# Kernel tuning notes

Measured on AMD Instinct MI355X. Metric: run time of the kernel, lower is better.

Reference implementation:

```python
import jax, jax.numpy as jnp
import numpy as np

EMBED_DIM = 1024
NUM_HEADS = 16
HEAD_DIM = EMBED_DIM // NUM_HEADS
B, T = 4, 2048


def setup_inputs() -> dict:
    key = jax.random.key(0)
    ks = jax.random.split(key, 10)
    s = 1.0 / np.sqrt(EMBED_DIM)
    inp = {
        "x": jax.random.normal(ks[0], (B, T, EMBED_DIM), dtype=jnp.float32),
        "mask": jnp.ones((B, T), dtype=bool),
        "q_w": jax.random.uniform(ks[1], (EMBED_DIM, EMBED_DIM), jnp.float32, -s, s),
        "q_b": jax.random.uniform(ks[2], (EMBED_DIM,), jnp.float32, -s, s),
        "k_w": jax.random.uniform(ks[3], (EMBED_DIM, EMBED_DIM), jnp.float32, -s, s),
        "k_b": jax.random.uniform(ks[4], (EMBED_DIM,), jnp.float32, -s, s),
        "v_w": jax.random.uniform(ks[5], (EMBED_DIM, EMBED_DIM), jnp.float32, -s, s),
        "v_b": jax.random.uniform(ks[6], (EMBED_DIM,), jnp.float32, -s, s),
        "o_w": jax.random.uniform(ks[7], (EMBED_DIM, EMBED_DIM), jnp.float32, -s, s),
        "o_b": jax.random.uniform(ks[8], (EMBED_DIM,), jnp.float32, -s, s),
    }
    return inp


def reference(x, mask, q_w, q_b, k_w, k_b, v_w, v_b, o_w, o_b):
    # NOTE: original module accepts `mask` but never uses it; dropout defined but never applied.
    Bn, Tn, C = x.shape
    H, D = NUM_HEADS, HEAD_DIM
    # Linear: x @ W.T + b, then split heads -> [B, H, T, D]
    Q = (x @ q_w.T + q_b).reshape(Bn, Tn, H, D).transpose(0, 2, 1, 3)
    K = (x @ k_w.T + k_b).reshape(Bn, Tn, H, D).transpose(0, 2, 1, 3)
    V = (x @ v_w.T + v_b).reshape(Bn, Tn, H, D).transpose(0, 2, 1, 3)
    scores = jnp.einsum("bhqd,bhkd->bhqk", Q, K) / jnp.sqrt(jnp.float32(D))
    attn = jax.nn.softmax(scores, axis=-1)
    out = jnp.einsum("bhqk,bhkd->bhqd", attn, V)
    out = out.transpose(0, 2, 1, 3).reshape(Bn, Tn, C)
    return out @ o_w.T + o_b
```

## Files before the change

kernel.cpp:

```cpp
#include <hip/hip_runtime.h>
#include <stdint.h>

#define B_ 4
#define T_ 2048
#define C_ 1024
#define H_ 16
#define D_ 64
#define CK 1024

typedef __attribute__((ext_vector_type(8))) short bf8;
typedef __attribute__((ext_vector_type(4))) float f4;

__device__ __forceinline__ ushort f2bf(float f) {
  union { float f; uint32_t u; } c; c.f = f;
  uint32_t u = c.u;
  uint32_t r = (u + 0x7fffu + ((u >> 16) & 1u)) >> 16;
  return (ushort)r;
}

__device__ __forceinline__ uint32_t cvtpk(float a, float b) {
  uint32_t r;
  asm("v_cvt_pk_bf16_f32 %0, %1, %2" : "=v"(r) : "v"(a), "v"(b));
  return r;
}

__global__ __launch_bounds__(256) void cast_f32_bf16(const float* __restrict__ in,
                                                     ushort* __restrict__ out, int n) {
  int i = (blockIdx.x * 256 + threadIdx.x) * 4;
  if (i >= n) return;
  float4 v = *(const float4*)(in + i);
  ushort4 o;
  o.x = f2bf(v.x); o.y = f2bf(v.y); o.z = f2bf(v.z); o.w = f2bf(v.w);
  *(ushort4*)(out + i) = o;
}

__global__ __launch_bounds__(256) void cast4_w(const float* __restrict__ w0,
                                               const float* __restrict__ w1,
                                               const float* __restrict__ w2,
                                               const float* __restrict__ w3,
                                               ushort* __restrict__ o0,
                                               ushort* __restrict__ o1,
                                               ushort* __restrict__ o2,
                                               ushort* __restrict__ o3) {
  const float* in;
  ushort* out;
  switch (blockIdx.y) {
    case 0: in = w0; out = o0; break;
    case 1: in = w1; out = o1; break;
    case 2: in = w2; out = o2; break;
    default: in = w3; out = o3; break;
  }
  int i = (blockIdx.x * 256 + threadIdx.x) * 4;
  float4 v = *(const float4*)(in + i);
  ushort4 o;
  o.x = f2bf(v.x); o.y = f2bf(v.y); o.z = f2bf(v.z); o.w = f2bf(v.w);
  *(ushort4*)(out + i) = o;
}

__global__ __launch_bounds__(256) void transpose_v(const ushort* __restrict__ in,
                                                   ushort* __restrict__ out) {
  __shared__ ushort tile[64 * 65];
  const int tid = threadIdx.x;
  const int bh = blockIdx.y, t0 = blockIdx.x * 64;
  const int r = tid >> 3, c8 = (tid & 7) * 8;

  const ushort* src = in + ((size_t)bh * T_ + t0 + r) * D_ + c8;
  *(int4*)&tile[r * 65 + c8]        = *(const int4*)&src[0];
  *(int4*)&tile[(r + 32) * 65 + c8] = *(const int4*)&src[32 * D_];
  __syncthreads();

#pragma unroll
  for (int p = 0; p < 2; ++p) {
    int d = p * 32 + (tid >> 3), tc = (tid & 7) * 8;
    ushort tmp[8];
#pragma unroll
    for (int i = 0; i < 8; ++i) tmp[i] = tile[(tc + i) * 65 + d];
    *(int4*)&out[((size_t)bh * D_ + d) * T_ + t0 + tc] = *(int4*)tmp;
  }
}

__global__ __launch_bounds__(512, 2) void gemm8(const ushort* __restrict__ A,
                                                const ushort* __restrict__ W,
                                                const float* __restrict__ b0,
                                                const float* __restrict__ b1,
                                                const float* __restrict__ b2,
                                                void* __restrict__ outp,
                                                int mode, float qsc) {
  extern __shared__ ushort smem[];
  ushort* sA = smem;
  ushort* sB = smem + 16384;

  const int tid = threadIdx.x;
  const int w = tid >> 6, l = tid & 63, lo = l & 15, hi = l >> 4;
  const int wm = w >> 2, wn = w & 3;

  const int i = blockIdx.x;
  const int m0 = ((i & 7) * 8 + ((i >> 3) & 7)) * 128;
  const int n0 = (i >> 6) * 256;

  const int rl = tid >> 3, c7 = tid & 7;
  const int scol = (c7 ^ (rl & 7)) * 8;
  const ushort* Asrc = A + (size_t)(m0 + rl) * CK + scol;
  const int Brow0 = ((rl >> 5) * 64) + (rl & 31);
  const ushort* Bsrc = W + (size_t)(n0 + Brow0) * CK + scol;
  const int Bdst0 = Brow0 * 64 + c7 * 8;

  const int sw0 = (hi ^ (lo & 7)) * 8;
  const int sw1 = ((4 + hi) ^ (lo & 7)) * 8;
  const int arow = wm * 64 + lo;
  const int brow = wn * 64 + lo;

  f4 acc[4][4];
#pragma unroll
  for (int f = 0; f < 4; ++f)
#pragma unroll
    for (int g = 0; g < 4; ++g) acc[f][g] = (f4){0.f, 0.f, 0.f, 0.f};

#define GL(src, dst) __builtin_amdgcn_global_load_lds(                                   \
      (const __attribute__((address_space(1))) void*)(src),                              \
      (__attribute__((address_space(3))) void*)(dst), 16, 0, 0)
#define STG_A(nb, kn) {                                                                  \
    GL(Asrc + (kn),                    &sA[(nb)*8192 + tid*8]);                          \
    GL(Asrc + (kn) + (size_t)64 * CK,  &sA[(nb)*8192 + 4096 + tid*8]); }
#define STG_B(nb, h, kn) {                                                               \
    GL(Bsrc + (kn) + (size_t)((h)*32) * CK,        &sB[(nb)*16384 + (h)*2048 + Bdst0]);           \
    GL(Bsrc + (kn) + (size_t)((h)*32 + 128) * CK,  &sB[(nb)*16384 + (h)*2048 + 8192 + Bdst0]); }
#define VMC(s)  asm volatile("s_waitcnt vmcnt(" s ")" ::: "memory")
#define PH_BAR  { __builtin_amdgcn_s_barrier(); asm volatile("" ::: "memory"); }
#define LDA(cb) {                                                                        \
  _Pragma("unroll")                                                                      \
  for (int f = 0; f < 4; ++f) {                                                          \
    af[f][0] = *(const bf8*)&sA[(cb)*8192 + (arow + f*16)*64 + sw0];                     \
    af[f][1] = *(const bf8*)&sA[(cb)*8192 + (arow + f*16)*64 + sw1]; } }
#define LDB(cb, dst, h) {                                                                \
  _Pragma("unroll")                                                                      \
  for (int g = 0; g < 2; ++g) {                                                          \
    dst[g][0] = *(const bf8*)&sB[(cb)*16384 + (brow + (h)*32 + g*16)*64 + sw0];          \
    dst[g][1] = *(const bf8*)&sB[(cb)*16384 + (brow + (h)*32 + g*16)*64 + sw1]; } }
#define MM(h, bfr) {                                                                     \
  __builtin_amdgcn_s_setprio(1);                                                         \
  _Pragma("unroll")                                                                      \
  for (int f = 0; f < 4; ++f)                                                            \
    _Pragma("unroll")                                                                    \
    for (int g = 0; g < 2; ++g) {                                                        \
      acc[f][(h)*2+g] = __builtin_amdgcn_mfma_f32_16x16x32_bf16(af[f][0], bfr[g][0], acc[f][(h)*2+g], 0, 0, 0); \
      acc[f][(h)*2+g] = __builtin_amdgcn_mfma_f32_16x16x32_bf16(af[f][1], bfr[g][1], acc[f][(h)*2+g], 0, 0, 0); } \
  __builtin_amdgcn_s_setprio(0); }

  bf8 af[4][2], bA[2][2], bB[2][2];

  STG_A(0, 0); STG_B(0, 0, 0); STG_B(0, 1, 0);
  VMC("0"); PH_BAR;
  int cur = 0;

  for (int t = 0; t < (CK / 64) - 1; ++t) {
    const int nb = cur ^ 1;
    const int kn = (t + 1) * 64;
    LDA(cur); LDB(cur, bA, 0);
    STG_A(nb, kn); STG_B(nb, 0, kn);
    VMC("6"); PH_BAR;
    MM(0, bA); PH_BAR;
    LDB(cur, bB, 1);
    STG_B(nb, 1, kn);
    VMC("6"); PH_BAR;
    MM(1, bB); PH_BAR;
    cur = nb;
  }
  VMC("0"); PH_BAR;
  LDA(cur); LDB(cur, bA, 0); MM(0, bA);
  LDB(cur, bB, 1);           MM(1, bB);
#undef GL
#undef STG_A
#undef STG_B
#undef VMC
#undef PH_BAR
#undef LDA
#undef LDB
#undef MM

  if (mode == 0) {
    float* O = (float*)outp;
#pragma unroll
    for (int f = 0; f < 4; ++f)
#pragma unroll
      for (int gn = 0; gn < 4; ++gn) {
        int n = n0 + wn * 64 + gn * 16 + lo;
        float bv = b0[n];
#pragma unroll
        for (int j = 0; j < 4; ++j) {
          int m = m0 + wm * 64 + f * 16 + hi * 4 + j;
          O[(size_t)m * C_ + n] = acc[f][gn][j] + bv;
        }
      }
  } else {
    const int proj = n0 >> 10;
    const float* bp = (proj == 0) ? b0 : ((proj == 1) ? b1 : b2);
    const float os = (proj == 0) ? qsc : 1.0f;
    ushort* O = (ushort*)outp + (size_t)proj * (8u << 20);
#pragma unroll
    for (int f = 0; f < 4; ++f)
#pragma unroll
      for (int gn = 0; gn < 4; ++gn) {
        int n = n0 + wn * 64 + gn * 16 + lo;
        int nl = n & 1023;
        int h = nl >> 6, d = n & 63;
        float bv = bp[nl];
#pragma unroll
        for (int j = 0; j < 4; ++j) {
          int m = m0 + wm * 64 + f * 16 + hi * 4 + j;
          int b = m >> 11, t = m & 2047;
          O[(size_t)((b << 4) + h) * (T_ * D_) + t * D_ + d] = f2bf((acc[f][gn][j] + bv) * os);
        }
      }
  }
}

__global__ __launch_bounds__(256, 4) void attn_kernel(const ushort* __restrict__ Q,
                                                      const ushort* __restrict__ Kg,
                                                      const ushort* __restrict__ VT,
                                                      ushort* __restrict__ O) {
  __shared__ ushort Ks[2][64 * 64];
  __shared__ ushort Vs[2][64 * 64];

  const int tid = threadIdx.x;
  const int w = tid >> 6, l = tid & 63, lo = l & 15, hi = l >> 4;
  const int linear = blockIdx.y * 16 + blockIdx.x;
  const int bh = (linear & 7) * 8 + ((linear >> 3) & 7);
  const int q0 = (linear >> 6) * 128 + w * 32;
  const ushort* Qb  = Q  + (size_t)bh * T_ * D_;
  const ushort* Kb  = Kg + (size_t)bh * T_ * D_;
  const ushort* VTb = VT + (size_t)bh * D_ * T_;

  bf8 qf[2][2];
#pragma unroll
  for (int qs = 0; qs < 2; ++qs)
#pragma unroll
    for (int c = 0; c < 2; ++c)
      qf[qs][c] = *(const bf8*)&Qb[(q0 + qs * 16 + lo) * D_ + c * 32 + hi * 8];

  f4 o[2][4], accL[2];
#pragma unroll
  for (int qs = 0; qs < 2; ++qs) {
    accL[qs] = (f4){0.f, 0.f, 0.f, 0.f};
#pragma unroll
    for (int dt = 0; dt < 4; ++dt) o[qs][dt] = (f4){0.f, 0.f, 0.f, 0.f};
  }
  const short ONE = 0x3F80;
  const bf8 ones = (bf8){ONE, ONE, ONE, ONE, ONE, ONE, ONE, ONE};

  const int rowA  = tid >> 3;
  const int colsw = ((tid & 7) ^ (rowA & 7)) * 8;
  const int permA = ((rowA >> 2) & 3) * 8 + ((rowA >> 4) & 1) * 4 + (rowA & 3);
  const ushort* Ksrc0 = Kb  + (size_t)permA * D_ + colsw;
  const ushort* Ksrc1 = Kb  + (size_t)(32 + permA) * D_ + colsw;
  const ushort* Vsrc0 = VTb + (size_t)rowA * T_ + colsw;
  const ushort* Vsrc1 = VTb + (size_t)(rowA + 32) * T_ + colsw;

  const int swz = (lo & 7) << 3;
  const int NT = T_ / 64;

#define STAGE(b, kvo)                                                                              \
  {                                                                                                \
    __builtin_amdgcn_global_load_lds((const __attribute__((address_space(1))) void*)(Ksrc0 + (size_t)(kvo) * D_), \
                                     (__attribute__((address_space(3))) void*)&Ks[b][tid * 8], 16, 0, 0);          \
    __builtin_amdgcn_global_load_lds((const __attribute__((address_space(1))) void*)(Ksrc1 + (size_t)(kvo) * D_), \
                                     (__attribute__((address_space(3))) void*)&Ks[b][2048 + tid * 8], 16, 0, 0);   \
    __builtin_amdgcn_global_load_lds((const __attribute__((address_space(1))) void*)(Vsrc0 + (kvo)),               \
                                     (__attribute__((address_space(3))) void*)&Vs[b][tid * 8], 16, 0, 0);          \
    __builtin_amdgcn_global_load_lds((const __attribute__((address_space(1))) void*)(Vsrc1 + (kvo)),               \
                                     (__attribute__((address_space(3))) void*)&Vs[b][2048 + tid * 8], 16, 0, 0);   \
  }

  STAGE(0, 0);
  __syncthreads();
  int cur = 0;

  for (int t = 0; t < NT; ++t) {
    if (t + 1 < NT) STAGE(cur ^ 1, (t + 1) * 64);

    const ushort* Kc = &Ks[cur][0];
    const ushort* Vc = &Vs[cur][0];

    bf8 kf[4][2], vf[4][2];
#pragma unroll
    for (int n = 0; n < 4; ++n) {
      kf[n][0] = *(const bf8*)&Kc[(n * 16 + lo) * 64 + ((hi * 8) ^ swz)];
      kf[n][1] = *(const bf8*)&Kc[(n * 16 + lo) * 64 + ((32 + hi * 8) ^ swz)];
    }
#pragma unroll
    for (int dt = 0; dt < 4; ++dt) {
      vf[dt][0] = *(const bf8*)&Vc[(dt * 16 + lo) * 64 + ((hi * 8) ^ swz)];
      vf[dt][1] = *(const bf8*)&Vc[(dt * 16 + lo) * 64 + ((32 + hi * 8) ^ swz)];
    }

#pragma unroll
    for (int qs = 0; qs < 2; ++qs) {
      f4 z[4];
#pragma unroll
      for (int n = 0; n < 4; ++n) {
        f4 zz = (f4){0.f, 0.f, 0.f, 0.f};
        zz = __builtin_amdgcn_mfma_f32_16x16x32_bf16(kf[n][0], qf[qs][0], zz, 0, 0, 0);
        zz = __builtin_amdgcn_mfma_f32_16x16x32_bf16(kf[n][1], qf[qs][1], zz, 0, 0, 0);
        z[n] = zz;
      }

      uint32_t pd[8];
#pragma unroll
      for (int n = 0; n < 4; ++n) {
        float e0 = __builtin_amdgcn_exp2f(z[n][0]);
        float e1 = __builtin_amdgcn_exp2f(z[n][1]);
        float e2 = __builtin_amdgcn_exp2f(z[n][2]);
        float e3 = __builtin_amdgcn_exp2f(z[n][3]);
        pd[n * 2 + 0] = cvtpk(e0, e1);
        pd[n * 2 + 1] = cvtpk(e2, e3);
      }
      union U8 { uint32_t u[4]; bf8 v; } u0, u1;
      u0.u[0] = pd[0]; u0.u[1] = pd[1]; u0.u[2] = pd[2]; u0.u[3] = pd[3];
      u1.u[0] = pd[4]; u1.u[1] = pd[5]; u1.u[2] = pd[6]; u1.u[3] = pd[7];

      accL[qs] = __builtin_amdgcn_mfma_f32_16x16x32_bf16(u0.v, ones, accL[qs], 0, 0, 0);
      accL[qs] = __builtin_amdgcn_mfma_f32_16x16x32_bf16(u1.v, ones, accL[qs], 0, 0, 0);

#pragma unroll
      for (int dt = 0; dt < 4; ++dt) {
        o[qs][dt] = __builtin_amdgcn_mfma_f32_16x16x32_bf16(u0.v, vf[dt][0], o[qs][dt], 0, 0, 0);
        o[qs][dt] = __builtin_amdgcn_mfma_f32_16x16x32_bf16(u1.v, vf[dt][1], o[qs][dt], 0, 0, 0);
      }
    }

    __syncthreads();
    cur ^= 1;
  }
#undef STAGE

  const int b = bh >> 4, h = bh & 15;
#pragma unroll
  for (int qs = 0; qs < 2; ++qs)
#pragma unroll
    for (int j = 0; j < 4; ++j) {
      float invL = 1.0f / accL[qs][j];
      int q = q0 + qs * 16 + hi * 4 + j;
#pragma unroll
      for (int dt = 0; dt < 4; ++dt)
        O[(size_t)(b * T_ + q) * C_ + h * D_ + dt * 16 + lo] = f2bf(o[qs][dt][j] * invL);
    }
}

extern "C" void kernel_launch(void* const* d_in, const int* in_sizes, int n_in,
                              void* d_out, int out_size, void* d_ws, size_t ws_size,
                              hipStream_t stream) {
  const float* x  = (const float*)d_in[0];
  const float* qw = (const float*)d_in[2];
  const float* qb = (const float*)d_in[3];
  const float* kw = (const float*)d_in[4];
  const float* kb = (const float*)d_in[5];
  const float* vw = (const float*)d_in[6];
  const float* vb = (const float*)d_in[7];
  const float* ow = (const float*)d_in[8];
  const float* ob = (const float*)d_in[9];
  float* out = (float*)d_out;

  char* ws = (char*)d_ws;
  ushort* xbf   = (ushort*)ws;
  ushort* VTws  = (ushort*)ws;
  ushort* qwbf  = (ushort*)(ws + (16u << 20));
  ushort* kwbf  = qwbf + (1u << 20);
  ushort* vwbf  = kwbf + (1u << 20);
  ushort* owbf  = vwbf + (1u << 20);
  ushort* Qws   = (ushort*)(ws + (24u << 20));
  ushort* Vws   = (ushort*)(ws + (56u << 20));
  ushort* attnw = (ushort*)(ws + (72u << 20));

  hipFuncSetAttribute((const void*)gemm8, hipFuncAttributeMaxDynamicSharedMemorySize, 98304);

  const int NX = B_ * T_ * C_;
  const int NW = C_ * C_;
  cast_f32_bf16<<<NX / 4 / 256, 256, 0, stream>>>(x, xbf, NX);
  cast4_w<<<dim3(NW / 4 / 256, 4), 256, 0, stream>>>(qw, kw, vw, ow, qwbf, kwbf, vwbf, owbf);

  const float QSC = 0.125f * 1.44269504f;
  gemm8<<<768, 512, 98304, stream>>>(xbf, qwbf, qb, kb, vb, Qws, 1, QSC);

  transpose_v<<<dim3(T_ / 64, B_ * H_), 256, 0, stream>>>(Vws, VTws);

  attn_kernel<<<dim3(T_ / 128, B_ * H_), 256, 0, stream>>>(Qws, Qws + (size_t)(8u << 20), VTws, attnw);

  gemm8<<<256, 512, 98304, stream>>>(attnw, owbf, ob, nullptr, nullptr, out, 0, 1.0f);
}
```

Measured before the change: 174.2 us.

## Fuse V transpose into QKV GEMM epilogue and unroll attention double-buffer loop

The QKV projection epilogue now writes the V projection directly in transposed [bh][d][t] layout using packed 4-element stores, so the separate transpose_v kernel and its round trip through memory are removed. The attention main loop is manually unrolled by two with fixed buffer indices, which removes the runtime buffer toggling. It also wraps the PV MFMAs in s_setprio to favour the matrix issue. The transposed V stores are strided across d, which may reduce write coalescing in the GEMM epilogue.

```diff
diff --git a/kernel.cpp b/kernel.cpp
--- a/kernel.cpp
+++ b/kernel.cpp
@@ -55,28 +55,6 @@
   ushort4 o;
   o.x = f2bf(v.x); o.y = f2bf(v.y); o.z = f2bf(v.z); o.w = f2bf(v.w);
   *(ushort4*)(out + i) = o;
-}
-
-__global__ __launch_bounds__(256) void transpose_v(const ushort* __restrict__ in,
-                                                   ushort* __restrict__ out) {
-  __shared__ ushort tile[64 * 65];
-  const int tid = threadIdx.x;
-  const int bh = blockIdx.y, t0 = blockIdx.x * 64;
-  const int r = tid >> 3, c8 = (tid & 7) * 8;
-
-  const ushort* src = in + ((size_t)bh * T_ + t0 + r) * D_ + c8;
-  *(int4*)&tile[r * 65 + c8]        = *(const int4*)&src[0];
-  *(int4*)&tile[(r + 32) * 65 + c8] = *(const int4*)&src[32 * D_];
-  __syncthreads();
-
-#pragma unroll
-  for (int p = 0; p < 2; ++p) {
-    int d = p * 32 + (tid >> 3), tc = (tid & 7) * 8;
-    ushort tmp[8];
-#pragma unroll
-    for (int i = 0; i < 8; ++i) tmp[i] = tile[(tc + i) * 65 + d];
-    *(int4*)&out[((size_t)bh * D_ + d) * T_ + t0 + tc] = *(int4*)tmp;
-  }
 }
 
 __global__ __launch_bounds__(512, 2) void gemm8(const ushort* __restrict__ A,
@@ -194,24 +172,45 @@
       }
   } else {
     const int proj = n0 >> 10;
-    const float* bp = (proj == 0) ? b0 : ((proj == 1) ? b1 : b2);
-    const float os = (proj == 0) ? qsc : 1.0f;
-    ushort* O = (ushort*)outp + (size_t)proj * (8u << 20);
-#pragma unroll
-    for (int f = 0; f < 4; ++f)
-#pragma unroll
-      for (int gn = 0; gn < 4; ++gn) {
-        int n = n0 + wn * 64 + gn * 16 + lo;
-        int nl = n & 1023;
-        int h = nl >> 6, d = n & 63;
-        float bv = bp[nl];
-#pragma unroll
-        for (int j = 0; j < 4; ++j) {
-          int m = m0 + wm * 64 + f * 16 + hi * 4 + j;
-          int b = m >> 11, t = m & 2047;
-          O[(size_t)((b << 4) + h) * (T_ * D_) + t * D_ + d] = f2bf((acc[f][gn][j] + bv) * os);
+    if (proj < 2) {
+      const float* bp = (proj == 0) ? b0 : b1;
+      const float os = (proj == 0) ? qsc : 1.0f;
+      ushort* O = (ushort*)outp + (size_t)proj * (8u << 20);
+#pragma unroll
+      for (int f = 0; f < 4; ++f)
+#pragma unroll
+        for (int gn = 0; gn < 4; ++gn) {
+          int n = n0 + wn * 64 + gn * 16 + lo;
+          int nl = n & 1023;
+          int h = nl >> 6, d = nl & 63;
+          float bv = bp[nl];
+#pragma unroll
+          for (int j = 0; j < 4; ++j) {
+            int m = m0 + wm * 64 + f * 16 + hi * 4 + j;
+            int b = m >> 11, t = m & 2047;
+            O[(size_t)((b << 4) + h) * (T_ * D_) + t * D_ + d] = f2bf((acc[f][gn][j] + bv) * os);
+          }
         }
-      }
+    } else {
+      ushort* O = (ushort*)outp + (size_t)2 * (8u << 20);
+#pragma unroll
+      for (int f = 0; f < 4; ++f)
+#pragma unroll
+        for (int gn = 0; gn < 4; ++gn) {
+          int n = n0 + wn * 64 + gn * 16 + lo;
+          int nl = n & 1023;
+          int h = nl >> 6, d = nl & 63;
+          float bv = b2[nl];
+          int mb = m0 + wm * 64 + f * 16 + hi * 4;
+          int b = mb >> 11, t = mb & 2047;
+          ushort4 pk;
+          pk.x = f2bf(acc[f][gn][0] + bv);
+          pk.y = f2bf(acc[f][gn][1] + bv);
+          pk.z = f2bf(acc[f][gn][2] + bv);
+          pk.w = f2bf(acc[f][gn][3] + bv);
+          *(ushort4*)&O[((size_t)((b << 4) + h) * D_ + d) * T_ + t] = pk;
+        }
+    }
   }
 }
 
@@ -271,67 +270,69 @@
                                      (__attribute__((address_space(3))) void*)&Vs[b][2048 + tid * 8], 16, 0, 0);   \
   }
 
+#define TILE(bb)                                                                                   \
+  {                                                                                                \
+    const ushort* Kc = &Ks[bb][0];                                                                 \
+    const ushort* Vc = &Vs[bb][0];                                                                 \
+    bf8 kf[4][2], vf[4][2];                                                                        \
+    _Pragma("unroll")                                                                              \
+    for (int n = 0; n < 4; ++n) {                                                                  \
+      kf[n][0] = *(const bf8*)&Kc[(n * 16 + lo) * 64 + ((hi * 8) ^ swz)];                          \
+      kf[n][1] = *(const bf8*)&Kc[(n * 16 + lo) * 64 + ((32 + hi * 8) ^ swz)];                     \
+    }                                                                                              \
+    _Pragma("unroll")                                                                              \
+    for (int dt = 0; dt < 4; ++dt) {                                                               \
+      vf[dt][0] = *(const bf8*)&Vc[(dt * 16 + lo) * 64 + ((hi * 8) ^ swz)];                        \
+      vf[dt][1] = *(const bf8*)&Vc[(dt * 16 + lo) * 64 + ((32 + hi * 8) ^ swz)];                   \
+    }                                                                                              \
+    _Pragma("unroll")                                                                              \
+    for (int qs = 0; qs < 2; ++qs) {                                                               \
+      f4 z[4];                                                                                     \
+      _Pragma("unroll")                                                                            \
+      for (int n = 0; n < 4; ++n) {                                                                \
+        f4 zz = (f4){0.f, 0.f, 0.f, 0.f};                                                          \
+        zz = __builtin_amdgcn_mfma_f32_16x16x32_bf16(kf[n][0], qf[qs][0], zz, 0, 0, 0);            \
+        zz = __builtin_amdgcn_mfma_f32_16x16x32_bf16(kf[n][1], qf[qs][1], zz, 0, 0, 0);            \
+        z[n] = zz;                                                                                 \
+      }                                                                                            \
+      uint32_t pd[8];                                                                              \
+      _Pragma("unroll")                                                                            \
+      for (int n = 0; n < 4; ++n) {                                                                \
+        float e0 = __builtin_amdgcn_exp2f(z[n][0]);                                                \
+        float e1 = __builtin_amdgcn_exp2f(z[n][1]);                                                \
+        float e2 = __builtin_amdgcn_exp2f(z[n][2]);                                                \
+        float e3 = __builtin_amdgcn_exp2f(z[n][3]);                                                \
+        pd[n * 2 + 0] = cvtpk(e0, e1);                                                             \
+        pd[n * 2 + 1] = cvtpk(e2, e3);                                                             \
+      }                                                                                            \
+      union U8 { uint32_t u[4]; bf8 v; } u0, u1;                                                   \
+      u0.u[0] = pd[0]; u0.u[1] = pd[1]; u0.u[2] = pd[2]; u0.u[3] = pd[3];                          \
+      u1.u[0] = pd[4]; u1.u[1] = pd[5]; u1.u[2] = pd[6]; u1.u[3] = pd[7];                          \
+      __builtin_amdgcn_s_setprio(1);                                                               \
+      accL[qs] = __builtin_amdgcn_mfma_f32_16x16x32_bf16(u0.v, ones, accL[qs], 0, 0, 0);           \
+      accL[qs] = __builtin_amdgcn_mfma_f32_16x16x32_bf16(u1.v, ones, accL[qs], 0, 0, 0);           \
+      _Pragma("unroll")                                                                            \
+      for (int dt = 0; dt < 4; ++dt) {                                                             \
+        o[qs][dt] = __builtin_amdgcn_mfma_f32_16x16x32_bf16(u0.v, vf[dt][0], o[qs][dt], 0, 0, 0);  \
+        o[qs][dt] = __builtin_amdgcn_mfma_f32_16x16x32_bf16(u1.v, vf[dt][1], o[qs][dt], 0, 0, 0);  \
+      }                                                                                            \
+      __builtin_amdgcn_s_setprio(0);                                                               \
+    }                                                                                              \
+  }
+
   STAGE(0, 0);
   __syncthreads();
-  int cur = 0;
-
-  for (int t = 0; t < NT; ++t) {
-    if (t + 1 < NT) STAGE(cur ^ 1, (t + 1) * 64);
-
-    const ushort* Kc = &Ks[cur][0];
-    const ushort* Vc = &Vs[cur][0];
-
-    bf8 kf[4][2], vf[4][2];
-#pragma unroll
-    for (int n = 0; n < 4; ++n) {
-      kf[n][0] = *(const bf8*)&Kc[(n * 16 + lo) * 64 + ((hi * 8) ^ swz)];
-      kf[n][1] = *(const bf8*)&Kc[(n * 16 + lo) * 64 + ((32 + hi * 8) ^ swz)];
-    }
-#pragma unroll
-    for (int dt = 0; dt < 4; ++dt) {
-      vf[dt][0] = *(const bf8*)&Vc[(dt * 16 + lo) * 64 + ((hi * 8) ^ swz)];
-      vf[dt][1] = *(const bf8*)&Vc[(dt * 16 + lo) * 64 + ((32 + hi * 8) ^ swz)];
-    }
-
-#pragma unroll
-    for (int qs = 0; qs < 2; ++qs) {
-      f4 z[4];
-#pragma unroll
-      for (int n = 0; n < 4; ++n) {
-        f4 zz = (f4){0.f, 0.f, 0.f, 0.f};
-        zz = __builtin_amdgcn_mfma_f32_16x16x32_bf16(kf[n][0], qf[qs][0], zz, 0, 0, 0);
-        zz = __builtin_amdgcn_mfma_f32_16x16x32_bf16(kf[n][1], qf[qs][1], zz, 0, 0, 0);
-        z[n] = zz;
-      }
-
-      uint32_t pd[8];
-#pragma unroll
-      for (int n = 0; n < 4; ++n) {
-        float e0 = __builtin_amdgcn_exp2f(z[n][0]);
-        float e1 = __builtin_amdgcn_exp2f(z[n][1]);
-        float e2 = __builtin_amdgcn_exp2f(z[n][2]);
-        float e3 = __builtin_amdgcn_exp2f(z[n][3]);
-        pd[n * 2 + 0] = cvtpk(e0, e1);
-        pd[n * 2 + 1] = cvtpk(e2, e3);
-      }
-      union U8 { uint32_t u[4]; bf8 v; } u0, u1;
-      u0.u[0] = pd[0]; u0.u[1] = pd[1]; u0.u[2] = pd[2]; u0.u[3] = pd[3];
-      u1.u[0] = pd[4]; u1.u[1] = pd[5]; u1.u[2] = pd[6]; u1.u[3] = pd[7];
-
-      accL[qs] = __builtin_amdgcn_mfma_f32_16x16x32_bf16(u0.v, ones, accL[qs], 0, 0, 0);
-      accL[qs] = __builtin_amdgcn_mfma_f32_16x16x32_bf16(u1.v, ones, accL[qs], 0, 0, 0);
-
-#pragma unroll
-      for (int dt = 0; dt < 4; ++dt) {
-        o[qs][dt] = __builtin_amdgcn_mfma_f32_16x16x32_bf16(u0.v, vf[dt][0], o[qs][dt], 0, 0, 0);
-        o[qs][dt] = __builtin_amdgcn_mfma_f32_16x16x32_bf16(u1.v, vf[dt][1], o[qs][dt], 0, 0, 0);
-      }
-    }
-
+
+  for (int t = 0; t < NT - 1; t += 2) {
+    STAGE(1, (t + 1) * 64);
+    TILE(0);
     __syncthreads();
-    cur ^= 1;
+    if (t + 2 < NT) STAGE(0, (t + 2) * 64);
+    TILE(1);
+    __syncthreads();
   }
 #undef STAGE
+#undef TILE
 
   const int b = bh >> 4, h = bh & 15;
 #pragma unroll
@@ -362,13 +363,12 @@
 
   char* ws = (char*)d_ws;
   ushort* xbf   = (ushort*)ws;
-  ushort* VTws  = (ushort*)ws;
   ushort* qwbf  = (ushort*)(ws + (16u << 20));
   ushort* kwbf  = qwbf + (1u << 20);
   ushort* vwbf  = kwbf + (1u << 20);
   ushort* owbf  = vwbf + (1u << 20);
   ushort* Qws   = (ushort*)(ws + (24u << 20));
-  ushort* Vws   = (ushort*)(ws + (56u << 20));
+  ushort* VTws  = (ushort*)(ws + (56u << 20));
   ushort* attnw = (ushort*)(ws + (72u << 20));
 
   hipFuncSetAttribute((const void*)gemm8, hipFuncAttributeMaxDynamicSharedMemorySize, 98304);
@@ -381,8 +381,6 @@
   const float QSC = 0.125f * 1.44269504f;
   gemm8<<<768, 512, 98304, stream>>>(xbf, qwbf, qb, kb, vb, Qws, 1, QSC);
 
-  transpose_v<<<dim3(T_ / 64, B_ * H_), 256, 0, stream>>>(Vws, VTws);
-
   attn_kernel<<<dim3(T_ / 128, B_ * H_), 256, 0, stream>>>(Qws, Qws + (size_t)(8u << 20), VTws, attnw);
 
   gemm8<<<256, 512, 98304, stream>>>(attnw, owbf, ob, nullptr, nullptr, out, 0, 1.0f);
```

Result: slower. 335.6 us (+92.6%).
